# Kernel optimization log

Hardware: AMD Instinct MI355X
Metric: run time of the kernel (lower is better)

The kernel has to match this reference:

```python
import jax, jax.numpy as jnp
import numpy as np

N = 100000
IN_DIM, H1, H2, OUT_DIM = 128, 128, 16, 10
DROP_P = 0.5


def setup_inputs() -> dict:
    key = jax.random.key(0)
    ks = jax.random.split(key, 9)
    x = jax.random.normal(ks[0], (N, IN_DIM), dtype=jnp.float32)
    edge_index = jax.random.randint(ks[1], (2, 1600000), 0, N, dtype=jnp.int64)
    s = lambda k, sh, fan: jax.random.normal(k, sh, jnp.float32) * (1.0 / np.sqrt(fan))
    return {
        "x": x,
        "edge_index": edge_index,
        "W1": s(ks[2], (IN_DIM, H1), IN_DIM),
        "b1": jnp.zeros((H1,), jnp.float32),
        "W2": s(ks[3], (H1, H2), H1),
        "b2": jnp.zeros((H2,), jnp.float32),
        "prelu_a": jnp.array(0.25, jnp.float32),  # nn.PReLU(): single shared parameter
        "Wfc": s(ks[4], (H2, OUT_DIM), H2),
        "bfc": jnp.zeros((OUT_DIM,), jnp.float32),
    }


def _prelu(x, a):
    return jnp.where(x >= 0, x, a * x)


def _dropout(x, key, p=DROP_P):
    keep = jax.random.bernoulli(key, 1.0 - p, x.shape)
    return jnp.where(keep, x / (1.0 - p), 0.0)


def _gcn_norm(edge_index, n):
    # PyG GCNConv default: add self-loops, symmetric deg^-1/2 normalization
    loop = jnp.arange(n, dtype=edge_index.dtype)
    src = jnp.concatenate([edge_index[0], loop])
    dst = jnp.concatenate([edge_index[1], loop])
    deg = jax.ops.segment_sum(jnp.ones_like(src, jnp.float32), dst, num_segments=n)
    dis = jnp.where(deg > 0, jax.lax.rsqrt(deg), 0.0)
    norm = dis[src] * dis[dst]  # [E + N]
    return src, dst, norm


def _gcn_conv(h, src, dst, norm, b, n):
    msg = h[src] * norm[:, None]          # gather + per-edge scale
    agg = jax.ops.segment_sum(msg, dst, num_segments=n)  # scatter-add
    return agg + b


def reference(x, edge_index, W1, b1, W2, b2, prelu_a, Wfc, bfc):
    n = x.shape[0]
    src, dst, norm = _gcn_norm(edge_index, n)
    dk1, dk2 = jax.random.split(jax.random.key(42))
    h = _gcn_conv(x @ W1, src, dst, norm, b1, n)
    h = _dropout(_prelu(h, prelu_a), dk1)
    h = _gcn_conv(h @ W2, src, dst, norm, b2, n)
    h = _dropout(_prelu(h, prelu_a), dk2)
    return h @ Wfc + bfc
```

## Files before the change

### kernel.cpp

```cpp
#include <hip/hip_runtime.h>
#include <stdint.h>

#define G1  128
#define BSH 9
#define BSZ 512

typedef __attribute__((ext_vector_type(8))) _Float16 f16x8;
typedef __attribute__((ext_vector_type(2))) _Float16 f16x2;
typedef __attribute__((ext_vector_type(2))) __fp16 fp16x2r;
typedef __attribute__((ext_vector_type(4))) float f32x4;

#define TF_ROUND(x0, x1, r)                                                    \
  {                                                                            \
    x0 += x1;                                                                  \
    x1 = (x1 << r) | (x1 >> (32 - r));                                         \
    x1 ^= x0;                                                                  \
  }

__host__ __device__ inline void threefry2x32(uint32_t k0, uint32_t k1,
                                             uint32_t x0, uint32_t x1,
                                             uint32_t* o0, uint32_t* o1) {
  uint32_t ks2 = k0 ^ k1 ^ 0x1BD11BDAu;
  x0 += k0; x1 += k1;
  TF_ROUND(x0, x1, 13) TF_ROUND(x0, x1, 15) TF_ROUND(x0, x1, 26) TF_ROUND(x0, x1, 6)
  x0 += k1; x1 += ks2 + 1u;
  TF_ROUND(x0, x1, 17) TF_ROUND(x0, x1, 29) TF_ROUND(x0, x1, 16) TF_ROUND(x0, x1, 24)
  x0 += ks2; x1 += k0 + 2u;
  TF_ROUND(x0, x1, 13) TF_ROUND(x0, x1, 15) TF_ROUND(x0, x1, 26) TF_ROUND(x0, x1, 6)
  x0 += k0; x1 += k1 + 3u;
  TF_ROUND(x0, x1, 17) TF_ROUND(x0, x1, 29) TF_ROUND(x0, x1, 16) TF_ROUND(x0, x1, 24)
  x0 += k1; x1 += ks2 + 4u;
  TF_ROUND(x0, x1, 13) TF_ROUND(x0, x1, 15) TF_ROUND(x0, x1, 26) TF_ROUND(x0, x1, 6)
  x0 += ks2; x1 += k0 + 5u;
  *o0 = x0; *o1 = x1;
}

__device__ inline uint32_t tf_bits32(uint32_t k0, uint32_t k1, uint32_t ctr) {
  uint32_t a, b;
  threefry2x32(k0, k1, 0u, ctr, &a, &b);
  return a ^ b;
}

__device__ inline f16x2 u2h(uint32_t u) {
  union { uint32_t u; f16x2 h; } c; c.u = u; return c.h;
}
__device__ inline uint32_t h2u(f16x2 h) {
  union { uint32_t u; f16x2 h; } c; c.h = h; return c.u;
}
__device__ inline uint32_t pk2h(float a, float b) {
  union { fp16x2r h; uint32_t u; } c;
  c.h = __builtin_amdgcn_cvt_pkrtz(a, b);
  return c.u;
}
__device__ inline uint16_t f2h(float a) {
  union { fp16x2r h; uint32_t u; } c;
  c.h = __builtin_amdgcn_cvt_pkrtz(a, 0.f);
  return (uint16_t)c.u;
}

__global__ __launch_bounds__(256) void k_build1(
    const int* __restrict__ dst, int* __restrict__ hist_t, int E, int NB, int chunk,
    const float* __restrict__ x, const float* __restrict__ W,
    uint16_t* __restrict__ h, int n) {
  __shared__ char smem[(64 * 136 + 128 * 136) * 2];
  const int tid = threadIdx.x;
  if (blockIdx.x < G1) {
    int* hist = (int*)smem;
    for (int b = tid; b < NB; b += 256) hist[b] = 0;
    __syncthreads();
    int e0 = blockIdx.x * chunk;
    int e1 = min(e0 + chunk, E);
    for (int e = e0 + tid; e < e1; e += 256)
      atomicAdd(&hist[dst[e] >> BSH], 1);
    __syncthreads();
    for (int b = tid; b < NB; b += 256)
      hist_t[b * G1 + blockIdx.x] = hist[b];
    return;
  }
  uint16_t (*As)[136] = (uint16_t(*)[136])smem;
  uint16_t (*Bs)[136] = (uint16_t(*)[136])(smem + 64 * 136 * 2);
  const int rowBase = (blockIdx.x - G1) * 64;
  for (int i = tid; i < 64 * 32; i += 256) {
    int r = i >> 5, c4 = i & 31;
    float4 v = make_float4(0.f, 0.f, 0.f, 0.f);
    if (rowBase + r < n)
      v = ((const float4*)(x + (size_t)(rowBase + r) * 128))[c4];
    *(uint2*)&As[r][c4 * 4] = make_uint2(pk2h(v.x, v.y), pk2h(v.z, v.w));
  }
  {
    int k2 = tid >> 7;
    int c = tid & 127;
    for (int kk = 0; kk < 128; kk += 4) {
      int k = kk + k2 * 2;
      *(uint32_t*)&Bs[c][k] = pk2h(W[k * 128 + c], W[(k + 1) * 128 + c]);
    }
  }
  __syncthreads();
  const int wid = tid >> 6;
  const int lane = tid & 63;
  const int l15 = lane & 15;
  const int lhi = lane >> 4;
  f32x4 acc[8];
#pragma unroll
  for (int t = 0; t < 8; ++t) acc[t] = (f32x4){0.f, 0.f, 0.f, 0.f};
  const int arow = wid * 16 + l15;
#pragma unroll
  for (int ks = 0; ks < 4; ++ks) {
    f16x8 a = *(f16x8*)&As[arow][ks * 32 + lhi * 8];
#pragma unroll
    for (int ct = 0; ct < 8; ++ct) {
      f16x8 bfrag = *(f16x8*)&Bs[ct * 16 + l15][ks * 32 + lhi * 8];
      acc[ct] = __builtin_amdgcn_mfma_f32_16x16x32_f16(a, bfrag, acc[ct], 0, 0, 0);
    }
  }
#pragma unroll
  for (int j = 0; j < 4; ++j) {
    int row = rowBase + wid * 16 + lhi * 4 + j;
    if (row < n) {
#pragma unroll
      for (int ct = 0; ct < 8; ++ct)
        h[(size_t)row * 128 + ct * 16 + l15] = f2h(acc[ct][j]);
    }
  }
}

__global__ __launch_bounds__(1024) void k_bscan(int* __restrict__ h, int T) {
  __shared__ int sh[1024];
  int per = (T + 1023) >> 10;
  int b0 = min((int)threadIdx.x * per, T);
  int b1 = min(b0 + per, T);
  int s = 0;
  for (int i = b0; i < b1; ++i) s += h[i];
  sh[threadIdx.x] = s;
  __syncthreads();
  for (int off = 1; off < 1024; off <<= 1) {
    int t = (threadIdx.x >= off) ? sh[threadIdx.x - off] : 0;
    __syncthreads();
    sh[threadIdx.x] += t;
    __syncthreads();
  }
  int run = sh[threadIdx.x] - s;
  for (int i = b0; i < b1; ++i) { int v = h[i]; h[i] = run; run += v; }
  if (threadIdx.x == 1023) h[T] = run;
}

__global__ __launch_bounds__(256) void k_bscatter(const int* __restrict__ src,
                                                  const int* __restrict__ dst,
                                                  const int* __restrict__ scanned,
                                                  uint32_t* __restrict__ ebuf,
                                                  int E, int NB, int chunk) {
  __shared__ int cur[256];
  int g = blockIdx.x;
  for (int b = threadIdx.x; b < NB; b += 256) cur[b] = scanned[b * G1 + g];
  __syncthreads();
  int e0 = g * chunk, e1 = min(e0 + chunk, E);
  for (int e = e0 + threadIdx.x; e < e1; e += 256) {
    int d = dst[e];
    int slot = atomicAdd(&cur[d >> BSH], 1);
    ebuf[slot] = ((uint32_t)src[e] << BSH) | (uint32_t)(d & (BSZ - 1));
  }
}

__global__ __launch_bounds__(256) void k_bfinal(const uint32_t* __restrict__ ebuf,
                                                const int* __restrict__ scanned,
                                                int* __restrict__ rowptr,
                                                float* __restrict__ dis,
                                                int* __restrict__ csrc,
                                                int n, int NB, int E) {
  __shared__ int cnt[BSZ];
  __shared__ int sc[256];
  int b = blockIdx.x;
  int t = threadIdx.x;
  int seg0 = scanned[b * G1];
  int seg1 = scanned[(b + 1) * G1];
  for (int i = t; i < BSZ; i += 256) cnt[i] = 0;
  __syncthreads();
  for (int i = seg0 + t; i < seg1; i += 256)
    atomicAdd(&cnt[ebuf[i] & (BSZ - 1)], 1);
  __syncthreads();
  int a0 = cnt[2 * t], a1 = cnt[2 * t + 1];
  int s = a0 + a1;
  sc[t] = s;
  __syncthreads();
  for (int off = 1; off < 256; off <<= 1) {
    int tmp = (t >= off) ? sc[t - off] : 0;
    __syncthreads();
    sc[t] += tmp;
    __syncthreads();
  }
  int pre = sc[t] - s;
  int node0 = b * BSZ;
  int p0 = seg0 + pre;
  int p1 = p0 + a0;
  int nd0 = node0 + 2 * t, nd1 = nd0 + 1;
  if (nd0 <= n) rowptr[nd0] = p0;
  if (nd1 <= n) rowptr[nd1] = p1;
  if (nd0 < n) dis[nd0] = rsqrtf((float)(a0 + 1));
  if (nd1 < n) dis[nd1] = rsqrtf((float)(a1 + 1));
  cnt[2 * t] = p0;
  cnt[2 * t + 1] = p1;
  __syncthreads();
  for (int i = seg0 + t; i < seg1; i += 256) {
    uint32_t u = ebuf[i];
    int slot = atomicAdd(&cnt[u & (BSZ - 1)], 1);
    csrc[slot] = (int)(u >> BSH);
  }
  if (b == NB - 1 && t == 0) rowptr[n] = E;
}

__global__ __launch_bounds__(256) void k_gather1(
    const int* __restrict__ rowptr, const int* __restrict__ csrc,
    const float* __restrict__ dis, const uint16_t* __restrict__ h1,
    const float* __restrict__ bias, const float* __restrict__ pa,
    uint32_t* __restrict__ outbuf, int n, uint32_t k0, uint32_t k1) {
  const int lane = threadIdx.x & 63;
  const int v = (blockIdx.x * blockDim.x + threadIdx.x) >> 6;
  if (v >= n) return;
  const int q = lane >> 4;
  const int sl = lane & 15;
  const int f0 = 8 * sl + 2 * q;
  uint32_t jj = (uint32_t)v * 128u + (uint32_t)f0;
  uint32_t bits0 = tf_bits32(k0, k1, jj);
  uint32_t bits1 = tf_bits32(k0, k1, jj + 1);
  float dv = dis[v];
  const uint4* rowbase = (const uint4*)h1;
  f16x2 acc0 = u2h(0u), acc1 = u2h(0u), acc2 = u2h(0u), acc3 = u2h(0u);
  if (q == 0) {
    uint4 r = rowbase[(size_t)v * 16 + sl];
    f16x2 w = u2h(pk2h(dv, dv));
    acc0 += u2h(r.x) * w; acc1 += u2h(r.y) * w;
    acc2 += u2h(r.z) * w; acc3 += u2h(r.w) * w;
  }
  int beg = rowptr[v];
  int deg = rowptr[v + 1] - beg;
  for (int base = 0; base < deg; base += 64) {
    int cnt = min(64, deg - base);
    int idx = base + lane;
    int sv = v;
    uint32_t wpk = 0u;
    if (idx < deg) {
      sv = csrc[beg + idx];
      float wd = dis[sv];
      wpk = pk2h(wd, wd);
    }
    for (int j = 0; j < cnt; j += 16) {
      int s0 = __shfl(sv, j + q);
      int s1 = __shfl(sv, j + 4 + q);
      int s2 = __shfl(sv, j + 8 + q);
      int s3 = __shfl(sv, j + 12 + q);
      uint32_t w0 = (uint32_t)__shfl((int)wpk, j + q);
      uint32_t w1 = (uint32_t)__shfl((int)wpk, j + 4 + q);
      uint32_t w2 = (uint32_t)__shfl((int)wpk, j + 8 + q);
      uint32_t w3 = (uint32_t)__shfl((int)wpk, j + 12 + q);
      uint4 r0 = rowbase[(size_t)s0 * 16 + sl];
      uint4 r1 = rowbase[(size_t)s1 * 16 + sl];
      uint4 r2 = rowbase[(size_t)s2 * 16 + sl];
      uint4 r3 = rowbase[(size_t)s3 * 16 + sl];
      f16x2 hw0 = u2h(w0), hw1 = u2h(w1), hw2 = u2h(w2), hw3 = u2h(w3);
      acc0 += u2h(r0.x) * hw0; acc1 += u2h(r0.y) * hw0;
      acc2 += u2h(r0.z) * hw0; acc3 += u2h(r0.w) * hw0;
      acc0 += u2h(r1.x) * hw1; acc1 += u2h(r1.y) * hw1;
      acc2 += u2h(r1.z) * hw1; acc3 += u2h(r1.w) * hw1;
      acc0 += u2h(r2.x) * hw2; acc1 += u2h(r2.y) * hw2;
      acc2 += u2h(r2.z) * hw2; acc3 += u2h(r2.w) * hw2;
      acc0 += u2h(r3.x) * hw3; acc1 += u2h(r3.y) * hw3;
      acc2 += u2h(r3.z) * hw3; acc3 += u2h(r3.w) * hw3;
    }
  }
#define COMB(A)                                                                \
  {                                                                            \
    uint32_t u_ = h2u(A);                                                      \
    A = A + u2h((uint32_t)__shfl_xor((int)u_, 16));                            \
    u_ = h2u(A);                                                               \
    A = A + u2h((uint32_t)__shfl_xor((int)u_, 32));                            \
  }
  COMB(acc0) COMB(acc1) COMB(acc2) COMB(acc3)
#undef COMB
  f16x2 p = (q == 0) ? acc0 : (q == 1) ? acc1 : (q == 2) ? acc2 : acc3;
  float a = pa[0];
  float v0 = (float)p.x * dv + bias[f0];
  float v1 = (float)p.y * dv + bias[f0 + 1];
  v0 = v0 >= 0.f ? v0 : a * v0;
  v1 = v1 >= 0.f ? v1 : a * v1;
  float r0 = (bits0 & 0x80000000u) ? 0.f : 2.f * v0;
  float r1 = (bits1 & 0x80000000u) ? 0.f : 2.f * v1;
  outbuf[(size_t)v * 64 + 4 * sl + q] = pk2h(r0, r1);
}

__global__ __launch_bounds__(256) void k_gemm2(const uint32_t* __restrict__ hbf,
                                               const float* __restrict__ W2,
                                               uint32_t* __restrict__ h2, int n) {
  __shared__ uint16_t As[64][136];
  __shared__ uint16_t Bs[16][136];
  const int tid = threadIdx.x;
  const int rowBase = blockIdx.x * 64;
  for (int i = tid; i < 64 * 32; i += 256) {
    int r = i >> 5, c4 = i & 31;
    uint2 v = make_uint2(0u, 0u);
    if (rowBase + r < n)
      v = ((const uint2*)(hbf + (size_t)(rowBase + r) * 64))[c4];
    *(uint2*)&As[r][c4 * 4] = v;
  }
  {
    int c = tid & 15;
    int k8 = tid >> 4;
#pragma unroll
    for (int jj = 0; jj < 8; ++jj) {
      int k = k8 * 8 + jj;
      Bs[c][k] = f2h(W2[k * 16 + c]);
    }
  }
  __syncthreads();
  const int wid = tid >> 6;
  const int lane = tid & 63;
  const int l15 = lane & 15;
  const int lhi = lane >> 4;
  f32x4 acc = (f32x4){0.f, 0.f, 0.f, 0.f};
  const int arow = wid * 16 + l15;
#pragma unroll
  for (int ks = 0; ks < 4; ++ks) {
    f16x8 a = *(f16x8*)&As[arow][ks * 32 + lhi * 8];
    f16x8 bfrag = *(f16x8*)&Bs[l15][ks * 32 + lhi * 8];
    acc = __builtin_amdgcn_mfma_f32_16x16x32_f16(a, bfrag, acc, 0, 0, 0);
  }
#pragma unroll
  for (int j = 0; j < 4; ++j) {
    int row = rowBase + wid * 16 + lhi * 4 + j;
    float val = (row < n) ? acc[j] : 0.f;
    float pv = __shfl_xor(val, 1);
    if (row < n && (l15 & 1) == 0)
      h2[(size_t)row * 8 + (l15 >> 1)] = pk2h(val, pv);
  }
}

__global__ __launch_bounds__(256) void k_gather2(
    const int* __restrict__ rowptr, const int* __restrict__ csrc,
    const float* __restrict__ dis, const uint32_t* __restrict__ h2,
    const float* __restrict__ bias, const float* __restrict__ pa,
    const float* __restrict__ Wfc, const float* __restrict__ bfc,
    float* __restrict__ out, int n, uint32_t k0, uint32_t k1) {
  __shared__ float wfc[16][10];
  __shared__ float sbfc[10];
  __shared__ float sval[32][16];
  const int tid = threadIdx.x;
  if (tid < 160) ((float*)wfc)[tid] = Wfc[tid];
  if (tid < 10) sbfc[tid] = bfc[tid];
  __syncthreads();
  int gnode = (blockIdx.x * 256 + tid) >> 3;
  int sub = tid & 7;
  int grp = tid >> 3;
  if (gnode < n) {
    float dv = dis[gnode];
    f16x2 acc = u2h(h2[(size_t)gnode * 8 + sub]) * u2h(pk2h(dv, dv));
    int beg = rowptr[gnode];
    int deg = rowptr[gnode + 1] - beg;
    for (int base = 0; base < deg; base += 8) {
      int cnt = min(8, deg - base);
      int idx = base + sub;
      int sv = gnode;
      uint32_t wpk = 0u;
      if (idx < deg) {
        sv = csrc[beg + idx];
        float wd = dis[sv];
        wpk = pk2h(wd, wd);
      }
      for (int j = 0; j < cnt; j += 4) {
        int s0 = __shfl(sv, j, 8);
        int s1 = __shfl(sv, j + 1, 8);
        int s2 = __shfl(sv, j + 2, 8);
        int s3 = __shfl(sv, j + 3, 8);
        uint32_t w0 = (uint32_t)__shfl((int)wpk, j, 8);
        uint32_t w1 = (uint32_t)__shfl((int)wpk, j + 1, 8);
        uint32_t w2 = (uint32_t)__shfl((int)wpk, j + 2, 8);
        uint32_t w3 = (uint32_t)__shfl((int)wpk, j + 3, 8);
        uint32_t r0 = h2[(size_t)s0 * 8 + sub];
        uint32_t r1 = h2[(size_t)s1 * 8 + sub];
        uint32_t r2 = h2[(size_t)s2 * 8 + sub];
        uint32_t r3 = h2[(size_t)s3 * 8 + sub];
        acc += u2h(r0) * u2h(w0);
        acc += u2h(r1) * u2h(w1);
        acc += u2h(r2) * u2h(w2);
        acc += u2h(r3) * u2h(w3);
      }
    }
    float a = pa[0];
    int kf = sub * 2;
    float v0 = (float)acc.x * dv + bias[kf];
    float v1 = (float)acc.y * dv + bias[kf + 1];
    v0 = v0 >= 0.f ? v0 : a * v0;
    v1 = v1 >= 0.f ? v1 : a * v1;
    uint32_t c0 = (uint32_t)gnode * 16u + (uint32_t)kf;
    uint32_t bits0 = tf_bits32(k0, k1, c0);
    uint32_t bits1 = tf_bits32(k0, k1, c0 + 1);
    sval[grp][kf]     = (bits0 & 0x80000000u) ? 0.f : 2.f * v0;
    sval[grp][kf + 1] = (bits1 & 0x80000000u) ? 0.f : 2.f * v1;
  }
  __syncthreads();
  if (gnode < n && sub < 5) {
    int c = sub * 2;
    float o0 = sbfc[c], o1 = sbfc[c + 1];
#pragma unroll
    for (int k = 0; k < 16; ++k) {
      float hv = sval[grp][k];
      o0 += hv * wfc[k][c];
      o1 += hv * wfc[k][c + 1];
    }
    *(float2*)&out[(size_t)gnode * 10 + c] = make_float2(o0, o1);
  }
}

extern "C" void kernel_launch(void* const* d_in, const int* in_sizes, int n_in,
                              void* d_out, int out_size, void* d_ws, size_t ws_size,
                              hipStream_t stream) {
  const float* x   = (const float*)d_in[0];
  const int*   ei  = (const int*)d_in[1];
  const float* W1  = (const float*)d_in[2];
  const float* b1  = (const float*)d_in[3];
  const float* W2  = (const float*)d_in[4];
  const float* b2  = (const float*)d_in[5];
  const float* pa  = (const float*)d_in[6];
  const float* Wfc = (const float*)d_in[7];
  const float* bfc = (const float*)d_in[8];
  float* out = (float*)d_out;

  const int n = in_sizes[0] / 128;
  const int E = in_sizes[1] / 2;
  const int* src = ei;
  const int* dst = ei + E;

  const int NB = (n + BSZ - 1) / BSZ;
  const int T = NB * G1;
  const int chunk = (E + G1 - 1) / G1;

  char* w = (char*)d_ws;
  auto alloc = [&](size_t bytes) {
    char* p = w;
    w += (bytes + 255) & ~(size_t)255;
    return p;
  };
  float* dis      = (float*)alloc((size_t)n * 4);
  int* rowptr     = (int*)alloc((size_t)(n + 1) * 4);
  int* hist_t     = (int*)alloc((size_t)(T + 1) * 4);
  uint32_t* ebuf  = (uint32_t*)alloc((size_t)E * 4);
  int* csrc       = (int*)alloc((size_t)E * 4);
  uint16_t* h1f   = (uint16_t*)alloc((size_t)n * 128 * 2);
  uint32_t* hbf   = (uint32_t*)alloc((size_t)n * 64 * 4);
  uint32_t* h2f   = (uint32_t*)alloc((size_t)n * 8 * 4);

  uint32_t dk1_0, dk1_1, dk2_0, dk2_1;
  threefry2x32(0u, 42u, 0u, 0u, &dk1_0, &dk1_1);
  threefry2x32(0u, 42u, 0u, 1u, &dk2_0, &dk2_1);

  k_build1<<<G1 + (n + 63) / 64, 256, 0, stream>>>(dst, hist_t, E, NB, chunk,
                                                   x, W1, h1f, n);
  k_bscan<<<1, 1024, 0, stream>>>(hist_t, T);
  k_bscatter<<<G1, 256, 0, stream>>>(src, dst, hist_t, ebuf, E, NB, chunk);
  k_bfinal<<<NB, 256, 0, stream>>>(ebuf, hist_t, rowptr, dis, csrc, n, NB, E);

  k_gather1<<<(n * 64 + 255) / 256, 256, 0, stream>>>(rowptr, csrc, dis, h1f,
                                                      b1, pa, hbf, n, dk1_0, dk1_1);

  k_gemm2<<<(n + 63) / 64, 256, 0, stream>>>(hbf, W2, h2f, n);

  k_gather2<<<(n * 8 + 255) / 256, 256, 0, stream>>>(rowptr, csrc, dis, h2f,
                                                     b2, pa, Wfc, bfc, out, n,
                                                     dk2_0, dk2_1);
}
```

Measured before the change: 205.2 us.

## Fuse layer-1 gather with GEMM2 and fold bucket scan into scatter

Removes the single-block scan kernel: each scatter block now computes its own bucket offsets by summing histogram rows and doing a block-level prefix scan, and block 0 writes per-bucket segment starts for the finalize kernel. Also fuses the layer-1 aggregation/PReLU/dropout with the W2 GEMM: each block aggregates 16 nodes (4 per wave), stages the fp16 result in shared memory, and one wave runs an MFMA against W2, so the 128-wide intermediate is never written to global memory. In exchange, every scatter block redundantly reads the full histogram, and the gather blocks process nodes serially per wave with a barrier and a single-wave GEMM tail, which may cut parallelism and latency hiding.

```diff
diff --git a/kernel.cpp b/kernel.cpp
--- a/kernel.cpp
+++ b/kernel.cpp
@@ -124,37 +124,40 @@
   }
 }
 
-__global__ __launch_bounds__(1024) void k_bscan(int* __restrict__ h, int T) {
-  __shared__ int sh[1024];
-  int per = (T + 1023) >> 10;
-  int b0 = min((int)threadIdx.x * per, T);
-  int b1 = min(b0 + per, T);
-  int s = 0;
-  for (int i = b0; i < b1; ++i) s += h[i];
-  sh[threadIdx.x] = s;
-  __syncthreads();
-  for (int off = 1; off < 1024; off <<= 1) {
-    int t = (threadIdx.x >= off) ? sh[threadIdx.x - off] : 0;
-    __syncthreads();
-    sh[threadIdx.x] += t;
-    __syncthreads();
-  }
-  int run = sh[threadIdx.x] - s;
-  for (int i = b0; i < b1; ++i) { int v = h[i]; h[i] = run; run += v; }
-  if (threadIdx.x == 1023) h[T] = run;
-}
-
-__global__ __launch_bounds__(256) void k_bscatter(const int* __restrict__ src,
-                                                  const int* __restrict__ dst,
-                                                  const int* __restrict__ scanned,
-                                                  uint32_t* __restrict__ ebuf,
-                                                  int E, int NB, int chunk) {
+__global__ __launch_bounds__(256) void k_bscatter(
+    const int* __restrict__ src, const int* __restrict__ dst,
+    const int* __restrict__ hist_t, int* __restrict__ segs,
+    uint32_t* __restrict__ ebuf, int E, int NB, int chunk) {
+  __shared__ int rowsum[256];
   __shared__ int cur[256];
-  int g = blockIdx.x;
-  for (int b = threadIdx.x; b < NB; b += 256) cur[b] = scanned[b * G1 + g];
+  const int g = blockIdx.x;
+  const int t = threadIdx.x;
+  int rs = 0, ps = 0;
+  if (t < NB) {
+    const int* row = hist_t + t * G1;
+    for (int i = 0; i < G1; ++i) {
+      int v = row[i];
+      rs += v;
+      if (i < g) ps += v;
+    }
+  }
+  rowsum[t] = rs;
+  __syncthreads();
+  for (int off = 1; off < 256; off <<= 1) {
+    int tmp = (t >= off) ? rowsum[t - off] : 0;
+    __syncthreads();
+    rowsum[t] += tmp;
+    __syncthreads();
+  }
+  int rb = rowsum[t] - rs;
+  if (t < NB) cur[t] = rb + ps;
+  if (g == 0) {
+    if (t < NB) segs[t] = rb;
+    if (t == 255) segs[NB] = rowsum[255];
+  }
   __syncthreads();
   int e0 = g * chunk, e1 = min(e0 + chunk, E);
-  for (int e = e0 + threadIdx.x; e < e1; e += 256) {
+  for (int e = e0 + t; e < e1; e += 256) {
     int d = dst[e];
     int slot = atomicAdd(&cur[d >> BSH], 1);
     ebuf[slot] = ((uint32_t)src[e] << BSH) | (uint32_t)(d & (BSZ - 1));
@@ -162,7 +165,7 @@
 }
 
 __global__ __launch_bounds__(256) void k_bfinal(const uint32_t* __restrict__ ebuf,
-                                                const int* __restrict__ scanned,
+                                                const int* __restrict__ segs,
                                                 int* __restrict__ rowptr,
                                                 float* __restrict__ dis,
                                                 int* __restrict__ csrc,
@@ -171,8 +174,8 @@
   __shared__ int sc[256];
   int b = blockIdx.x;
   int t = threadIdx.x;
-  int seg0 = scanned[b * G1];
-  int seg1 = scanned[(b + 1) * G1];
+  int seg0 = segs[b];
+  int seg1 = segs[b + 1];
   for (int i = t; i < BSZ; i += 256) cnt[i] = 0;
   __syncthreads();
   for (int i = seg0 + t; i < seg1; i += 256)
@@ -208,65 +211,85 @@
   if (b == NB - 1 && t == 0) rowptr[n] = E;
 }
 
-__global__ __launch_bounds__(256) void k_gather1(
+__global__ __launch_bounds__(256) void k_gather12(
     const int* __restrict__ rowptr, const int* __restrict__ csrc,
     const float* __restrict__ dis, const uint16_t* __restrict__ h1,
     const float* __restrict__ bias, const float* __restrict__ pa,
-    uint32_t* __restrict__ outbuf, int n, uint32_t k0, uint32_t k1) {
-  const int lane = threadIdx.x & 63;
-  const int v = (blockIdx.x * blockDim.x + threadIdx.x) >> 6;
-  if (v >= n) return;
+    const float* __restrict__ W2, uint32_t* __restrict__ h2,
+    int n, uint32_t k0, uint32_t k1) {
+  __shared__ uint16_t hs[16][136];
+  __shared__ uint16_t Bs[16][136];
+  const int tid = threadIdx.x;
+  {
+    int c = tid & 15;
+    int k8 = tid >> 4;
+#pragma unroll
+    for (int jj = 0; jj < 8; ++jj) {
+      int k = k8 * 8 + jj;
+      Bs[c][k] = f2h(W2[k * 16 + c]);
+    }
+  }
+  const int wid = tid >> 6;
+  const int lane = tid & 63;
   const int q = lane >> 4;
   const int sl = lane & 15;
   const int f0 = 8 * sl + 2 * q;
-  uint32_t jj = (uint32_t)v * 128u + (uint32_t)f0;
-  uint32_t bits0 = tf_bits32(k0, k1, jj);
-  uint32_t bits1 = tf_bits32(k0, k1, jj + 1);
-  float dv = dis[v];
+  const int base = blockIdx.x * 16;
   const uint4* rowbase = (const uint4*)h1;
-  f16x2 acc0 = u2h(0u), acc1 = u2h(0u), acc2 = u2h(0u), acc3 = u2h(0u);
-  if (q == 0) {
-    uint4 r = rowbase[(size_t)v * 16 + sl];
-    f16x2 w = u2h(pk2h(dv, dv));
-    acc0 += u2h(r.x) * w; acc1 += u2h(r.y) * w;
-    acc2 += u2h(r.z) * w; acc3 += u2h(r.w) * w;
-  }
-  int beg = rowptr[v];
-  int deg = rowptr[v + 1] - beg;
-  for (int base = 0; base < deg; base += 64) {
-    int cnt = min(64, deg - base);
-    int idx = base + lane;
-    int sv = v;
-    uint32_t wpk = 0u;
-    if (idx < deg) {
-      sv = csrc[beg + idx];
-      float wd = dis[sv];
-      wpk = pk2h(wd, wd);
-    }
-    for (int j = 0; j < cnt; j += 16) {
-      int s0 = __shfl(sv, j + q);
-      int s1 = __shfl(sv, j + 4 + q);
-      int s2 = __shfl(sv, j + 8 + q);
-      int s3 = __shfl(sv, j + 12 + q);
-      uint32_t w0 = (uint32_t)__shfl((int)wpk, j + q);
-      uint32_t w1 = (uint32_t)__shfl((int)wpk, j + 4 + q);
-      uint32_t w2 = (uint32_t)__shfl((int)wpk, j + 8 + q);
-      uint32_t w3 = (uint32_t)__shfl((int)wpk, j + 12 + q);
-      uint4 r0 = rowbase[(size_t)s0 * 16 + sl];
-      uint4 r1 = rowbase[(size_t)s1 * 16 + sl];
-      uint4 r2 = rowbase[(size_t)s2 * 16 + sl];
-      uint4 r3 = rowbase[(size_t)s3 * 16 + sl];
-      f16x2 hw0 = u2h(w0), hw1 = u2h(w1), hw2 = u2h(w2), hw3 = u2h(w3);
-      acc0 += u2h(r0.x) * hw0; acc1 += u2h(r0.y) * hw0;
-      acc2 += u2h(r0.z) * hw0; acc3 += u2h(r0.w) * hw0;
-      acc0 += u2h(r1.x) * hw1; acc1 += u2h(r1.y) * hw1;
-      acc2 += u2h(r1.z) * hw1; acc3 += u2h(r1.w) * hw1;
-      acc0 += u2h(r2.x) * hw2; acc1 += u2h(r2.y) * hw2;
-      acc2 += u2h(r2.z) * hw2; acc3 += u2h(r2.w) * hw2;
-      acc0 += u2h(r3.x) * hw3; acc1 += u2h(r3.y) * hw3;
-      acc2 += u2h(r3.z) * hw3; acc3 += u2h(r3.w) * hw3;
-    }
-  }
+  const float a = pa[0];
+  const float bi0 = bias[f0];
+  const float bi1 = bias[f0 + 1];
+  for (int i = 0; i < 4; ++i) {
+    const int nrow = wid * 4 + i;
+    const int v = base + nrow;
+    if (v < n) {
+      uint32_t jj = (uint32_t)v * 128u + (uint32_t)f0;
+      uint32_t bits0 = tf_bits32(k0, k1, jj);
+      uint32_t bits1 = tf_bits32(k0, k1, jj + 1);
+      float dv = dis[v];
+      f16x2 acc0 = u2h(0u), acc1 = u2h(0u), acc2 = u2h(0u), acc3 = u2h(0u);
+      if (q == 0) {
+        uint4 r = rowbase[(size_t)v * 16 + sl];
+        f16x2 w = u2h(pk2h(dv, dv));
+        acc0 += u2h(r.x) * w; acc1 += u2h(r.y) * w;
+        acc2 += u2h(r.z) * w; acc3 += u2h(r.w) * w;
+      }
+      int beg = rowptr[v];
+      int deg = rowptr[v + 1] - beg;
+      for (int bb = 0; bb < deg; bb += 64) {
+        int cnt = min(64, deg - bb);
+        int idx = bb + lane;
+        int sv = v;
+        uint32_t wpk = 0u;
+        if (idx < deg) {
+          sv = csrc[beg + idx];
+          float wd = dis[sv];
+          wpk = pk2h(wd, wd);
+        }
+        for (int j = 0; j < cnt; j += 16) {
+          int s0 = __shfl(sv, j + q);
+          int s1 = __shfl(sv, j + 4 + q);
+          int s2 = __shfl(sv, j + 8 + q);
+          int s3 = __shfl(sv, j + 12 + q);
+          uint32_t w0 = (uint32_t)__shfl((int)wpk, j + q);
+          uint32_t w1 = (uint32_t)__shfl((int)wpk, j + 4 + q);
+          uint32_t w2 = (uint32_t)__shfl((int)wpk, j + 8 + q);
+          uint32_t w3 = (uint32_t)__shfl((int)wpk, j + 12 + q);
+          uint4 r0 = rowbase[(size_t)s0 * 16 + sl];
+          uint4 r1 = rowbase[(size_t)s1 * 16 + sl];
+          uint4 r2 = rowbase[(size_t)s2 * 16 + sl];
+          uint4 r3 = rowbase[(size_t)s3 * 16 + sl];
+          f16x2 hw0 = u2h(w0), hw1 = u2h(w1), hw2 = u2h(w2), hw3 = u2h(w3);
+          acc0 += u2h(r0.x) * hw0; acc1 += u2h(r0.y) * hw0;
+          acc2 += u2h(r0.z) * hw0; acc3 += u2h(r0.w) * hw0;
+          acc0 += u2h(r1.x) * hw1; acc1 += u2h(r1.y) * hw1;
+          acc2 += u2h(r1.z) * hw1; acc3 += u2h(r1.w) * hw1;
+          acc0 += u2h(r2.x) * hw2; acc1 += u2h(r2.y) * hw2;
+          acc2 += u2h(r2.z) * hw2; acc3 += u2h(r2.w) * hw2;
+          acc0 += u2h(r3.x) * hw3; acc1 += u2h(r3.y) * hw3;
+          acc2 += u2h(r3.z) * hw3; acc3 += u2h(r3.w) * hw3;
+        }
+      }
 #define COMB(A)                                                                \
   {                                                                            \
     uint32_t u_ = h2u(A);                                                      \
@@ -274,62 +297,39 @@
     u_ = h2u(A);                                                               \
     A = A + u2h((uint32_t)__shfl_xor((int)u_, 32));                            \
   }
-  COMB(acc0) COMB(acc1) COMB(acc2) COMB(acc3)
+      COMB(acc0) COMB(acc1) COMB(acc2) COMB(acc3)
 #undef COMB
-  f16x2 p = (q == 0) ? acc0 : (q == 1) ? acc1 : (q == 2) ? acc2 : acc3;
-  float a = pa[0];
-  float v0 = (float)p.x * dv + bias[f0];
-  float v1 = (float)p.y * dv + bias[f0 + 1];
-  v0 = v0 >= 0.f ? v0 : a * v0;
-  v1 = v1 >= 0.f ? v1 : a * v1;
-  float r0 = (bits0 & 0x80000000u) ? 0.f : 2.f * v0;
-  float r1 = (bits1 & 0x80000000u) ? 0.f : 2.f * v1;
-  outbuf[(size_t)v * 64 + 4 * sl + q] = pk2h(r0, r1);
-}
-
-__global__ __launch_bounds__(256) void k_gemm2(const uint32_t* __restrict__ hbf,
-                                               const float* __restrict__ W2,
-                                               uint32_t* __restrict__ h2, int n) {
-  __shared__ uint16_t As[64][136];
-  __shared__ uint16_t Bs[16][136];
-  const int tid = threadIdx.x;
-  const int rowBase = blockIdx.x * 64;
-  for (int i = tid; i < 64 * 32; i += 256) {
-    int r = i >> 5, c4 = i & 31;
-    uint2 v = make_uint2(0u, 0u);
-    if (rowBase + r < n)
-      v = ((const uint2*)(hbf + (size_t)(rowBase + r) * 64))[c4];
-    *(uint2*)&As[r][c4 * 4] = v;
-  }
-  {
-    int c = tid & 15;
-    int k8 = tid >> 4;
-#pragma unroll
-    for (int jj = 0; jj < 8; ++jj) {
-      int k = k8 * 8 + jj;
-      Bs[c][k] = f2h(W2[k * 16 + c]);
-    }
-  }
-  __syncthreads();
-  const int wid = tid >> 6;
-  const int lane = tid & 63;
-  const int l15 = lane & 15;
-  const int lhi = lane >> 4;
-  f32x4 acc = (f32x4){0.f, 0.f, 0.f, 0.f};
-  const int arow = wid * 16 + l15;
-#pragma unroll
-  for (int ks = 0; ks < 4; ++ks) {
-    f16x8 a = *(f16x8*)&As[arow][ks * 32 + lhi * 8];
-    f16x8 bfrag = *(f16x8*)&Bs[l15][ks * 32 + lhi * 8];
-    acc = __builtin_amdgcn_mfma_f32_16x16x32_f16(a, bfrag, acc, 0, 0, 0);
-  }
-#pragma unroll
-  for (int j = 0; j < 4; ++j) {
-    int row = rowBase + wid * 16 + lhi * 4 + j;
-    float val = (row < n) ? acc[j] : 0.f;
-    float pv = __shfl_xor(val, 1);
-    if (row < n && (l15 & 1) == 0)
-      h2[(size_t)row * 8 + (l15 >> 1)] = pk2h(val, pv);
+      f16x2 p = (q == 0) ? acc0 : (q == 1) ? acc1 : (q == 2) ? acc2 : acc3;
+      float v0 = (float)p.x * dv + bi0;
+      float v1 = (float)p.y * dv + bi1;
+      v0 = v0 >= 0.f ? v0 : a * v0;
+      v1 = v1 >= 0.f ? v1 : a * v1;
+      float r0 = (bits0 & 0x80000000u) ? 0.f : 2.f * v0;
+      float r1 = (bits1 & 0x80000000u) ? 0.f : 2.f * v1;
+      *(uint32_t*)&hs[nrow][f0] = pk2h(r0, r1);
+    } else {
+      *(uint32_t*)&hs[nrow][f0] = 0u;
+    }
+  }
+  __syncthreads();
+  if (wid == 0) {
+    const int l15 = lane & 15;
+    const int lhi = lane >> 4;
+    f32x4 acc = (f32x4){0.f, 0.f, 0.f, 0.f};
+#pragma unroll
+    for (int ks = 0; ks < 4; ++ks) {
+      f16x8 af = *(f16x8*)&hs[l15][ks * 32 + lhi * 8];
+      f16x8 bf = *(f16x8*)&Bs[l15][ks * 32 + lhi * 8];
+      acc = __builtin_amdgcn_mfma_f32_16x16x32_f16(af, bf, acc, 0, 0, 0);
+    }
+#pragma unroll
+    for (int j = 0; j < 4; ++j) {
+      int gnode = base + lhi * 4 + j;
+      float val = acc[j];
+      float pv = __shfl_xor(val, 1);
+      if (gnode < n && (l15 & 1) == 0)
+        h2[(size_t)gnode * 8 + (l15 >> 1)] = pk2h(val, pv);
+    }
   }
 }
 
@@ -441,10 +441,10 @@
   float* dis      = (float*)alloc((size_t)n * 4);
   int* rowptr     = (int*)alloc((size_t)(n + 1) * 4);
   int* hist_t     = (int*)alloc((size_t)(T + 1) * 4);
+  int* segs       = (int*)alloc((size_t)(NB + 1) * 4);
   uint32_t* ebuf  = (uint32_t*)alloc((size_t)E * 4);
   int* csrc       = (int*)alloc((size_t)E * 4);
   uint16_t* h1f   = (uint16_t*)alloc((size_t)n * 128 * 2);
-  uint32_t* hbf   = (uint32_t*)alloc((size_t)n * 64 * 4);
   uint32_t* h2f   = (uint32_t*)alloc((size_t)n * 8 * 4);
 
   uint32_t dk1_0, dk1_1, dk2_0, dk2_1;
@@ -453,14 +453,11 @@
 
   k_build1<<<G1 + (n + 63) / 64, 256, 0, stream>>>(dst, hist_t, E, NB, chunk,
                                                    x, W1, h1f, n);
-  k_bscan<<<1, 1024, 0, stream>>>(hist_t, T);
-  k_bscatter<<<G1, 256, 0, stream>>>(src, dst, hist_t, ebuf, E, NB, chunk);
-  k_bfinal<<<NB, 256, 0, stream>>>(ebuf, hist_t, rowptr, dis, csrc, n, NB, E);
-
-  k_gather1<<<(n * 64 + 255) / 256, 256, 0, stream>>>(rowptr, csrc, dis, h1f,
-                                                      b1, pa, hbf, n, dk1_0, dk1_1);
-
-  k_gemm2<<<(n + 63) / 64, 256, 0, stream>>>(hbf, W2, h2f, n);
+  k_bscatter<<<G1, 256, 0, stream>>>(src, dst, hist_t, segs, ebuf, E, NB, chunk);
+  k_bfinal<<<NB, 256, 0, stream>>>(ebuf, segs, rowptr, dis, csrc, n, NB, E);
+
+  k_gather12<<<(n + 15) / 16, 256, 0, stream>>>(rowptr, csrc, dis, h1f,
+                                                b1, pa, W2, h2f, n, dk1_0, dk1_1);
 
   k_gather2<<<(n * 8 + 255) / 256, 256, 0, stream>>>(rowptr, csrc, dis, h2f,
                                                      b2, pa, Wfc, bfc, out, n,
```

New measurement: 170.9 us. 1.2x faster.
